# Kernel tuning notes

Measured on AMD Instinct MI355X. Metric: run time of the kernel, lower is better.

Reference implementation:

```python
import jax, jax.numpy as jnp
import numpy as np

# ---- static config (mirrors PointRend init kwargs) ----
H, W = 512, 512          # img_size
CH, CW = 128, 128        # coarse_size
FH, FW = 256, 256        # fine_size
CF = 256                 # fine_channels
NC = 3                   # num_classes (forced by MLP's hard-coded 259/131 channel counts)
NPTS = 2048              # N points
K_OVER = 3               # k oversampling
BELTA = 0.75
NUM_OVER = K_OVER * NPTS          # 6144
STEP1 = int(NPTS * BELTA)         # 1536 uncertain points
STEP2 = NPTS - STEP1              # 512 coverage points


def _xavier(key, c_out, c_in):
    std = (2.0 / (c_in + c_out)) ** 0.5
    return jax.random.normal(key, (c_out, c_in), jnp.float32) * std


def setup_inputs() -> dict:
    key = jax.random.key(0)
    k1, k2, k3, k4, k5, k6 = jax.random.split(key, 6)
    fine_grained = jax.random.normal(k1, (2, CF, FH, FW), jnp.float32)
    coarse_pre = jax.random.normal(k2, (2, NC, CH, CW), jnp.float32)
    # torch.randperm(H*W) done inside forward in the original; passed in for determinism
    random_1d_index = jax.random.permutation(k3, H * W).astype(jnp.int32)
    w1 = _xavier(k4, 256, CF + NC)   # conv1: 1x1, in=259, out=256, no bias
    w2 = _xavier(k5, 128, 256 + 3)   # conv2: in=259, out=128
    w3 = _xavier(k6, NC, 128 + 3)    # conv3: in=131, out=num_classes
    prelu_a = jnp.array(0.25, jnp.float32)  # shared single-param PReLU
    return dict(fine_grained=fine_grained, coarse_pre=coarse_pre,
                w1=w1, w2=w2, w3=w3, prelu_a=prelu_a,
                random_1d_index=random_1d_index)


def _bilinear(x, h, w):
    # matches nn.Upsample(mode='bilinear', align_corners=False)
    return jax.image.resize(x, (x.shape[0], x.shape[1], h, w), method="bilinear")


def _prelu(x, a):
    return jnp.where(x >= 0, x, a * x)


def _mlp(feat, w1, w2, w3, a):
    # feat: [B, N, C] -> channels-first [B, C, N]; BatchNorms in MLP are unused in forward.
    x = jnp.transpose(feat, (0, 2, 1))
    tail = x[:, -3:, :]  # last 3 channels appended to each layer's input
    l1 = _prelu(jnp.einsum('bcn,oc->bon', x, w1), a)
    l2 = _prelu(jnp.einsum('bcn,oc->bon', jnp.concatenate([l1, tail], 1), w2), a)
    return jnp.einsum('bcn,oc->bon', jnp.concatenate([l2, tail], 1), w3)  # [B, NC, N]


def reference(fine_grained, coarse_pre, w1, w2, w3, prelu_a, random_1d_index):
    B = fine_grained.shape[0]
    up_coarse_o = _bilinear(coarse_pre, H, W)            # [B, NC, H, W] logits
    up_coarse_sm = jax.nn.softmax(up_coarse_o, axis=1)   # softmax over classes
    up_fine = _bilinear(fine_grained, H, W)              # [B, CF, H, W]

    h_idx = random_1d_index // W
    w_idx = random_1d_index % W
    all_index = jnp.stack([h_idx, w_idx], axis=1)        # [H*W, 2]
    cand = all_index[:NUM_OVER]                          # oversampled candidates

    # vectorized replacement of the python loop: gather probs at candidates
    over_pre = up_coarse_sm[:, :, cand[:, 0], cand[:, 1]].transpose(0, 2, 1)  # [B, NUM_OVER, NC]
    top2, _ = jax.lax.top_k(over_pre, 2)
    uncertain = 1.0 - (top2[..., 0] - top2[..., 1])      # [B, NUM_OVER]
    _, u_idx = jax.lax.top_k(uncertain, STEP1)           # [B, STEP1]
    u_pts = cand[u_idx]                                  # [B, STEP1, 2]
    cov = jnp.broadcast_to(all_index[-STEP2:][None], (B, STEP2, 2))
    pts = jnp.concatenate([u_pts, cov], axis=1)          # [B, N, 2]

    # masked_select traverses the dense mask in row-major (h,w) order -> sort linear ids
    lin = pts[..., 0] * W + pts[..., 1]                  # [B, N]
    lin_sorted = jnp.sort(lin, axis=1)
    sh, sw = lin_sorted // W, lin_sorted % W
    bidx = jnp.arange(B)[:, None]
    sel_coarse = up_coarse_o[bidx, :, sh, sw]            # [B, N, NC] (pre-softmax feats)
    sel_fine = up_fine[bidx, :, sh, sw]                  # [B, N, CF]

    # faithful to torch: flat concat of the two masked_select outputs, then reshape
    feat = jnp.concatenate([sel_fine.reshape(-1), sel_coarse.reshape(-1)]).reshape(B, NPTS, -1)

    out = _mlp(feat, w1, w2, w3, prelu_a)                # [B, NC, N]
    mask = jnp.zeros((B, H, W), jnp.int32).at[bidx, pts[..., 0], pts[..., 1]].add(1)
    return out, mask
```

## Files before the change

### kernel.cpp

```cpp
#include <hip/hip_runtime.h>
#include <hip/hip_bf16.h>

#define NPTS 2048
#define NOVER 6144
#define STEP1 1536
#define STEP2 512
#define HW_TOT 262144

__device__ __forceinline__ float prelu_f(float x, float a) { return x >= 0.0f ? x : a * x; }

__device__ __forceinline__ void coarse_coords(int h, int w, float& fy, float& fx,
                                              int& y0, int& y1, int& x0, int& x1) {
  float sy = (h + 0.5f) * 0.25f - 0.5f;
  float sx = (w + 0.5f) * 0.25f - 0.5f;
  float yf = floorf(sy), xf = floorf(sx);
  fy = sy - yf; fx = sx - xf;
  int yi = (int)yf, xi = (int)xf;
  y0 = min(127, max(0, yi)); y1 = min(127, max(0, yi + 1));
  x0 = min(127, max(0, xi)); x1 = min(127, max(0, xi + 1));
}

__device__ __forceinline__ float coarse_sample(const float* __restrict__ ch, float fy, float fx,
                                               int y0, int y1, int x0, int x1) {
  float v00 = ch[(y0 << 7) + x0];
  float v01 = ch[(y0 << 7) + x1];
  float v10 = ch[(y1 << 7) + x0];
  float v11 = ch[(y1 << 7) + x1];
  return (1.0f - fy) * ((1.0f - fx) * v00 + fx * v01) + fy * ((1.0f - fx) * v10 + fx * v11);
}

__global__ __launch_bounds__(256) void pr_fill_v4(uint4* __restrict__ p) {
  p[blockIdx.x * 256 + threadIdx.x] = make_uint4(0u, 0u, 0u, 0u);
}

__global__ __launch_bounds__(256) void pr_wprep_v4(const float* __restrict__ w1,
                                                   const float* __restrict__ w2,
                                                   float* __restrict__ wT1,
                                                   float* __restrict__ wT2) {
  int gid = blockIdx.x * 256 + threadIdx.x;
  if (gid < 259 * 256) {
    int c = gid >> 8, o = gid & 255;
    wT1[c * 256 + o] = w1[o * 259 + c];
  } else {
    int g2 = gid - 259 * 256;
    if (g2 < 259 * 128) {
      int c = g2 >> 7, o = g2 & 127;
      wT2[c * 128 + o] = w2[o * 259 + c];
    }
  }
}

__global__ __launch_bounds__(256) void pr_uncert_v4(const float* __restrict__ coarse,
                                                    const int* __restrict__ ridx,
                                                    unsigned* __restrict__ keys) {
  int gid = blockIdx.x * 256 + threadIdx.x;
  if (gid >= 2 * NOVER) return;
  int b = gid / NOVER, i = gid - b * NOVER;
  int lin = ridx[i];
  int h = lin >> 9, w = lin & 511;
  float fy, fx; int y0, y1, x0, x1;
  coarse_coords(h, w, fy, fx, y0, y1, x0, x1);
  const float* cb = coarse + (((size_t)b * 3) << 14);
  float p0 = coarse_sample(cb, fy, fx, y0, y1, x0, x1);
  float p1 = coarse_sample(cb + (1 << 14), fy, fx, y0, y1, x0, x1);
  float p2 = coarse_sample(cb + (2 << 14), fy, fx, y0, y1, x0, x1);
  float m = fmaxf(p0, fmaxf(p1, p2));
  float e0 = expf(p0 - m), e1 = expf(p1 - m), e2 = expf(p2 - m);
  float s = e0 + e1 + e2;
  float q0 = e0 / s, q1 = e1 / s, q2 = e2 / s;
  float a0 = q0, a1 = q1, a2 = q2, tmp;
  if (a0 < a1) { tmp = a0; a0 = a1; a1 = tmp; }
  if (a1 < a2) { tmp = a1; a1 = a2; a2 = tmp; }
  if (a0 < a1) { tmp = a0; a0 = a1; a1 = tmp; }
  float u = 1.0f - (a0 - a1);
  keys[gid] = __float_as_uint(u);
}

__global__ __launch_bounds__(1024) void pr_topk_v4(const unsigned* __restrict__ keys,
                                                   const int* __restrict__ ridx,
                                                   int* __restrict__ lin_sorted,
                                                   float* __restrict__ mask) {
  __shared__ unsigned kv[NOVER];
  __shared__ unsigned bitmap[8192];
  __shared__ unsigned hist[256];
  __shared__ unsigned short tiebuf[NOVER];
  __shared__ unsigned scanbuf[16];
  __shared__ unsigned selinfo[2];
  __shared__ int tiecnt;
  const int b = blockIdx.x, t = threadIdx.x;
  const int lane = t & 63, wid = t >> 6;

  for (int i = t; i < NOVER; i += 1024) kv[i] = keys[b * NOVER + i];
  for (int i = t; i < 8192; i += 1024) bitmap[i] = 0u;
  if (t == 0) { selinfo[1] = STEP1; tiecnt = 0; }
  __syncthreads();

  unsigned prefix = 0u;
  for (int pass = 0; pass < 4; ++pass) {
    const int shift = 24 - 8 * pass;
    const unsigned maskHi = (pass == 0) ? 0u : (0xFFFFFFFFu << (shift + 8));
    for (int i = t; i < 256; i += 1024) hist[i] = 0u;
    __syncthreads();
    for (int i = t; i < NOVER; i += 1024) {
      unsigned k = kv[i];
      if ((k & maskHi) == prefix) atomicAdd(&hist[(k >> shift) & 255u], 1u);
    }
    __syncthreads();
    if (t < 64) {
      unsigned h0 = hist[t * 4], h1 = hist[t * 4 + 1], h2 = hist[t * 4 + 2], h3 = hist[t * 4 + 3];
      unsigned q = h0 + h1 + h2 + h3;
      unsigned s = q;
      for (int off = 1; off < 64; off <<= 1) {
        unsigned n = __shfl_down(s, off);
        if (t + off < 64) s += n;
      }
      unsigned exq = s - q;
      unsigned R = selinfo[1];
      unsigned se3 = exq, se2 = se3 + h3, se1 = se2 + h2, se0 = se1 + h1;
      if (se3 < R && R <= se3 + h3)      { selinfo[0] = prefix | ((unsigned)(t * 4 + 3) << shift); selinfo[1] = R - se3; }
      else if (se2 < R && R <= se2 + h2) { selinfo[0] = prefix | ((unsigned)(t * 4 + 2) << shift); selinfo[1] = R - se2; }
      else if (se1 < R && R <= se1 + h1) { selinfo[0] = prefix | ((unsigned)(t * 4 + 1) << shift); selinfo[1] = R - se1; }
      else if (se0 < R && R <= se0 + h0) { selinfo[0] = prefix | ((unsigned)(t * 4 + 0) << shift); selinfo[1] = R - se0; }
    }
    __syncthreads();
    prefix = selinfo[0];
  }
  const unsigned T = prefix;
  const int r = (int)selinfo[1];

  for (int i = t; i < NOVER; i += 1024) {
    unsigned k = kv[i];
    if (k > T) {
      int lin = ridx[i];
      mask[(size_t)b * HW_TOT + lin] = 1.0f;
      atomicOr(&bitmap[lin >> 5], 1u << (lin & 31));
    } else if (k == T) {
      int pos = atomicAdd(&tiecnt, 1);
      tiebuf[pos] = (unsigned short)i;
    }
  }
  for (int i = t; i < STEP2; i += 1024) {
    int lin = ridx[HW_TOT - STEP2 + i];
    mask[(size_t)b * HW_TOT + lin] = 1.0f;
    atomicOr(&bitmap[lin >> 5], 1u << (lin & 31));
  }
  __syncthreads();
  const int m = tiecnt;
  for (int j = t; j < m; j += 1024) {
    int idx = tiebuf[j];
    int rank = 0;
    for (int jj = 0; jj < m; ++jj) rank += (tiebuf[jj] < idx) ? 1 : 0;
    if (rank < r) {
      int lin = ridx[idx];
      mask[(size_t)b * HW_TOT + lin] = 1.0f;
      atomicOr(&bitmap[lin >> 5], 1u << (lin & 31));
    }
  }
  __syncthreads();

  unsigned mySum = 0;
#pragma unroll
  for (int q = 0; q < 8; ++q) mySum += __popc(bitmap[t * 8 + q]);
  unsigned v = mySum;
  for (int off = 1; off < 64; off <<= 1) {
    unsigned n = __shfl_up(v, off);
    if (lane >= off) v += n;
  }
  if (lane == 63) scanbuf[wid] = v;
  __syncthreads();
  if (t == 0) {
    unsigned run = 0;
    for (int w16 = 0; w16 < 16; ++w16) { unsigned tmp = scanbuf[w16]; scanbuf[w16] = run; run += tmp; }
  }
  __syncthreads();
  unsigned pos = (v - mySum) + scanbuf[wid];
  for (int q = 0; q < 8; ++q) {
    unsigned word = bitmap[t * 8 + q];
    int basebit = (t * 8 + q) << 5;
    while (word) {
      int bit = __ffs(word) - 1;
      word &= word - 1;
      lin_sorted[b * NPTS + pos++] = basebit + bit;
    }
  }
}

__global__ __launch_bounds__(256) void pr_mlp_v4(const float* __restrict__ fine,
                                                 const float* __restrict__ coarse,
                                                 const float* __restrict__ wT1,
                                                 const float* __restrict__ wT2,
                                                 const float* __restrict__ w3,
                                                 const float* __restrict__ pa,
                                                 const int* __restrict__ lin_sorted,
                                                 float* __restrict__ out) {
  __shared__ __align__(16) float xs[259][16];
  __shared__ __align__(16) float l1t[256][16];
  __shared__ __align__(16) float l2t[128][16];
  const int t = threadIdx.x;
  const int g0 = blockIdx.x * 16;
  const float a = pa[0];

  for (int task = t; task < 259 * 16; task += 256) {
    int c = task >> 4, p = task & 15;
    int g = g0 + p;
    int j = g * 259 + c;
    float v;
    if (j < 1048576) {
      int nsrc = j >> 8, ch = j & 255;
      int bs = nsrc >> 11;
      int lin = lin_sorted[nsrc];
      int h = lin >> 9, w = lin & 511;
      float sy = (h + 0.5f) * 0.5f - 0.5f;
      float sx = (w + 0.5f) * 0.5f - 0.5f;
      float yf = floorf(sy), xf = floorf(sx);
      float fy = sy - yf, fx = sx - xf;
      int yi = (int)yf, xi = (int)xf;
      int y0 = min(255, max(0, yi)), y1 = min(255, max(0, yi + 1));
      int x0 = min(255, max(0, xi)), x1 = min(255, max(0, xi + 1));
      const float* base = fine + (((size_t)(bs * 256 + ch)) << 16);
      float v00 = base[(y0 << 8) + x0];
      float v01 = base[(y0 << 8) + x1];
      float v10 = base[(y1 << 8) + x0];
      float v11 = base[(y1 << 8) + x1];
      v = (1.0f - fy) * ((1.0f - fx) * v00 + fx * v01) + fy * ((1.0f - fx) * v10 + fx * v11);
    } else {
      int jj = j - 1048576;
      int nsrc = jj / 3;
      int kk = jj - nsrc * 3;
      int bs = nsrc >> 11;
      int lin = lin_sorted[nsrc];
      int h = lin >> 9, w = lin & 511;
      float fy, fx; int y0, y1, x0, x1;
      coarse_coords(h, w, fy, fx, y0, y1, x0, x1);
      v = coarse_sample(coarse + (((size_t)bs * 3 + kk) << 14), fy, fx, y0, y1, x0, x1);
    }
    xs[c][p] = v;
  }
  __syncthreads();

  {
    const int ob = (t & 63) * 4;
    const int pb = (t >> 6) * 4;
    float acc[4][4];
#pragma unroll
    for (int i = 0; i < 4; ++i)
#pragma unroll
      for (int q = 0; q < 4; ++q) acc[i][q] = 0.0f;
    for (int c = 0; c < 259; ++c) {
      const float4 wv = *(const float4*)&wT1[c * 256 + ob];
      const float4 xv = *(const float4*)&xs[c][pb];
      acc[0][0] = fmaf(wv.x, xv.x, acc[0][0]); acc[0][1] = fmaf(wv.x, xv.y, acc[0][1]);
      acc[0][2] = fmaf(wv.x, xv.z, acc[0][2]); acc[0][3] = fmaf(wv.x, xv.w, acc[0][3]);
      acc[1][0] = fmaf(wv.y, xv.x, acc[1][0]); acc[1][1] = fmaf(wv.y, xv.y, acc[1][1]);
      acc[1][2] = fmaf(wv.y, xv.z, acc[1][2]); acc[1][3] = fmaf(wv.y, xv.w, acc[1][3]);
      acc[2][0] = fmaf(wv.z, xv.x, acc[2][0]); acc[2][1] = fmaf(wv.z, xv.y, acc[2][1]);
      acc[2][2] = fmaf(wv.z, xv.z, acc[2][2]); acc[2][3] = fmaf(wv.z, xv.w, acc[2][3]);
      acc[3][0] = fmaf(wv.w, xv.x, acc[3][0]); acc[3][1] = fmaf(wv.w, xv.y, acc[3][1]);
      acc[3][2] = fmaf(wv.w, xv.z, acc[3][2]); acc[3][3] = fmaf(wv.w, xv.w, acc[3][3]);
    }
#pragma unroll
    for (int i = 0; i < 4; ++i) {
      l1t[ob + i][pb + 0] = prelu_f(acc[i][0], a);
      l1t[ob + i][pb + 1] = prelu_f(acc[i][1], a);
      l1t[ob + i][pb + 2] = prelu_f(acc[i][2], a);
      l1t[ob + i][pb + 3] = prelu_f(acc[i][3], a);
    }
  }
  __syncthreads();

  {
    const int ob = (t & 31) * 4;
    const int pb = (t >> 5) * 2;
    float acc[4][2];
#pragma unroll
    for (int i = 0; i < 4; ++i) { acc[i][0] = 0.0f; acc[i][1] = 0.0f; }
    for (int c = 0; c < 256; ++c) {
      const float4 wv = *(const float4*)&wT2[c * 128 + ob];
      const float2 xv = *(const float2*)&l1t[c][pb];
      acc[0][0] = fmaf(wv.x, xv.x, acc[0][0]); acc[0][1] = fmaf(wv.x, xv.y, acc[0][1]);
      acc[1][0] = fmaf(wv.y, xv.x, acc[1][0]); acc[1][1] = fmaf(wv.y, xv.y, acc[1][1]);
      acc[2][0] = fmaf(wv.z, xv.x, acc[2][0]); acc[2][1] = fmaf(wv.z, xv.y, acc[2][1]);
      acc[3][0] = fmaf(wv.w, xv.x, acc[3][0]); acc[3][1] = fmaf(wv.w, xv.y, acc[3][1]);
    }
#pragma unroll
    for (int kk = 0; kk < 3; ++kk) {
      const float4 wv = *(const float4*)&wT2[(256 + kk) * 128 + ob];
      const float x0 = xs[256 + kk][pb], x1 = xs[256 + kk][pb + 1];
      acc[0][0] = fmaf(wv.x, x0, acc[0][0]); acc[0][1] = fmaf(wv.x, x1, acc[0][1]);
      acc[1][0] = fmaf(wv.y, x0, acc[1][0]); acc[1][1] = fmaf(wv.y, x1, acc[1][1]);
      acc[2][0] = fmaf(wv.z, x0, acc[2][0]); acc[2][1] = fmaf(wv.z, x1, acc[2][1]);
      acc[3][0] = fmaf(wv.w, x0, acc[3][0]); acc[3][1] = fmaf(wv.w, x1, acc[3][1]);
    }
#pragma unroll
    for (int i = 0; i < 4; ++i) {
      l2t[ob + i][pb + 0] = prelu_f(acc[i][0], a);
      l2t[ob + i][pb + 1] = prelu_f(acc[i][1], a);
    }
  }
  __syncthreads();

  if (t < 48) {
    const int o3 = t % 3, p = t / 3;
    const float* wr = w3 + o3 * 131;
    float s = 0.0f;
    for (int c = 0; c < 128; ++c) s = fmaf(wr[c], l2t[c][p], s);
#pragma unroll
    for (int kk = 0; kk < 3; ++kk) s = fmaf(wr[128 + kk], xs[256 + kk][p], s);
    const int g = g0 + p;
    out[((g >> 11) * 3 + o3) * 2048 + (g & 2047)] = s;
  }
}

extern "C" void kernel_launch(void* const* d_in, const int* in_sizes, int n_in,
                              void* d_out, int out_size, void* d_ws, size_t ws_size,
                              hipStream_t stream) {
  const float* fine   = (const float*)d_in[0];
  const float* coarse = (const float*)d_in[1];
  const float* w1     = (const float*)d_in[2];
  const float* w2     = (const float*)d_in[3];
  const float* w3     = (const float*)d_in[4];
  const float* pa     = (const float*)d_in[5];
  const int*   ridx   = (const int*)d_in[6];

  float* out  = (float*)d_out;
  float* mask = out + 2 * 3 * 2048;

  char* ws = (char*)d_ws;
  int*      lin_sorted = (int*)ws;
  float*    wT1  = (float*)(ws + 16384);
  float*    wT2  = (float*)(ws + 16384 + 265216);
  unsigned* keys = (unsigned*)(ws + 16384 + 265216 + 132608);

  pr_fill_v4<<<512, 256, 0, stream>>>((uint4*)mask);
  pr_wprep_v4<<<389, 256, 0, stream>>>(w1, w2, wT1, wT2);
  pr_uncert_v4<<<48, 256, 0, stream>>>(coarse, ridx, keys);
  pr_topk_v4<<<2, 1024, 0, stream>>>(keys, ridx, lin_sorted, mask);
  pr_mlp_v4<<<256, 256, 0, stream>>>(fine, coarse, wT1, wT2, w3, pa, lin_sorted, out);
}
```

Before: 254.8 us.

## Split feature gather into its own wide kernel before the MLP

Moves the bilinear gather of fine and coarse features out of the MLP kernel into a separate kernel launched with 4096 blocks that writes a dense feature buffer to workspace. The MLP kernel then loads its 16-point tile from that buffer. The aim is to spread the latency-bound scattered gathers across far more blocks than the 256-block MLP grid. The cost is an extra launch and a global round trip of about 4 MB of features.

```diff
diff --git a/kernel.cpp b/kernel.cpp
--- a/kernel.cpp
+++ b/kernel.cpp
@@ -29,11 +29,11 @@
   return (1.0f - fy) * ((1.0f - fx) * v00 + fx * v01) + fy * ((1.0f - fx) * v10 + fx * v11);
 }
 
-__global__ __launch_bounds__(256) void pr_fill_v4(uint4* __restrict__ p) {
+__global__ __launch_bounds__(256) void pr_fill_v5(uint4* __restrict__ p) {
   p[blockIdx.x * 256 + threadIdx.x] = make_uint4(0u, 0u, 0u, 0u);
 }
 
-__global__ __launch_bounds__(256) void pr_wprep_v4(const float* __restrict__ w1,
+__global__ __launch_bounds__(256) void pr_wprep_v5(const float* __restrict__ w1,
                                                    const float* __restrict__ w2,
                                                    float* __restrict__ wT1,
                                                    float* __restrict__ wT2) {
@@ -50,7 +50,7 @@
   }
 }
 
-__global__ __launch_bounds__(256) void pr_uncert_v4(const float* __restrict__ coarse,
+__global__ __launch_bounds__(256) void pr_uncert_v5(const float* __restrict__ coarse,
                                                     const int* __restrict__ ridx,
                                                     unsigned* __restrict__ keys) {
   int gid = blockIdx.x * 256 + threadIdx.x;
@@ -76,7 +76,7 @@
   keys[gid] = __float_as_uint(u);
 }
 
-__global__ __launch_bounds__(1024) void pr_topk_v4(const unsigned* __restrict__ keys,
+__global__ __launch_bounds__(1024) void pr_topk_v5(const unsigned* __restrict__ keys,
                                                    const int* __restrict__ ridx,
                                                    int* __restrict__ lin_sorted,
                                                    float* __restrict__ mask) {
@@ -185,24 +185,12 @@
   }
 }
 
-__global__ __launch_bounds__(256) void pr_mlp_v4(const float* __restrict__ fine,
-                                                 const float* __restrict__ coarse,
-                                                 const float* __restrict__ wT1,
-                                                 const float* __restrict__ wT2,
-                                                 const float* __restrict__ w3,
-                                                 const float* __restrict__ pa,
-                                                 const int* __restrict__ lin_sorted,
-                                                 float* __restrict__ out) {
-  __shared__ __align__(16) float xs[259][16];
-  __shared__ __align__(16) float l1t[256][16];
-  __shared__ __align__(16) float l2t[128][16];
-  const int t = threadIdx.x;
-  const int g0 = blockIdx.x * 16;
-  const float a = pa[0];
-
-  for (int task = t; task < 259 * 16; task += 256) {
-    int c = task >> 4, p = task & 15;
-    int g = g0 + p;
+__global__ __launch_bounds__(256) void pr_gather_v5(const float* __restrict__ fine,
+                                                    const float* __restrict__ coarse,
+                                                    const int* __restrict__ lin_sorted,
+                                                    float* __restrict__ feat) {
+  const int g = blockIdx.x;
+  for (int c = threadIdx.x; c < 259; c += 256) {
     int j = g * 259 + c;
     float v;
     if (j < 1048576) {
@@ -234,7 +222,28 @@
       coarse_coords(h, w, fy, fx, y0, y1, x0, x1);
       v = coarse_sample(coarse + (((size_t)bs * 3 + kk) << 14), fy, fx, y0, y1, x0, x1);
     }
-    xs[c][p] = v;
+    feat[j] = v;
+  }
+}
+
+__global__ __launch_bounds__(256) void pr_mlp_v5(const float* __restrict__ feat,
+                                                 const float* __restrict__ wT1,
+                                                 const float* __restrict__ wT2,
+                                                 const float* __restrict__ w3,
+                                                 const float* __restrict__ pa,
+                                                 float* __restrict__ out) {
+  __shared__ __align__(16) float xs[259][16];
+  __shared__ __align__(16) float l1t[256][16];
+  __shared__ __align__(16) float l2t[128][16];
+  const int t = threadIdx.x;
+  const int g0 = blockIdx.x * 16;
+  const float a = pa[0];
+
+  const float* fb = feat + g0 * 259;
+  for (int i = t; i < 16 * 259; i += 256) {
+    int p = i / 259;
+    int c = i - p * 259;
+    xs[c][p] = fb[i];
   }
   __syncthreads();
 
@@ -328,12 +337,14 @@
   char* ws = (char*)d_ws;
   int*      lin_sorted = (int*)ws;
   float*    wT1  = (float*)(ws + 16384);
-  float*    wT2  = (float*)(ws + 16384 + 265216);
-  unsigned* keys = (unsigned*)(ws + 16384 + 265216 + 132608);
-
-  pr_fill_v4<<<512, 256, 0, stream>>>((uint4*)mask);
-  pr_wprep_v4<<<389, 256, 0, stream>>>(w1, w2, wT1, wT2);
-  pr_uncert_v4<<<48, 256, 0, stream>>>(coarse, ridx, keys);
-  pr_topk_v4<<<2, 1024, 0, stream>>>(keys, ridx, lin_sorted, mask);
-  pr_mlp_v4<<<256, 256, 0, stream>>>(fine, coarse, wT1, wT2, w3, pa, lin_sorted, out);
-}
+  float*    wT2  = (float*)(ws + 281600);
+  unsigned* keys = (unsigned*)(ws + 414208);
+  float*    feat = (float*)(ws + 463360);
+
+  pr_fill_v5<<<512, 256, 0, stream>>>((uint4*)mask);
+  pr_wprep_v5<<<389, 256, 0, stream>>>(w1, w2, wT1, wT2);
+  pr_uncert_v5<<<48, 256, 0, stream>>>(coarse, ridx, keys);
+  pr_topk_v5<<<2, 1024, 0, stream>>>(keys, ridx, lin_sorted, mask);
+  pr_gather_v5<<<4096, 256, 0, stream>>>(fine, coarse, lin_sorted, feat);
+  pr_mlp_v5<<<256, 256, 0, stream>>>(feat, wT1, wT2, w3, pa, out);
+}
```

Result: slower. 260.8 us (+2.4%).
